# Kernel tuning notes

Measured on AMD Instinct MI355X. Metric: run time of the kernel, lower is better.

The kernel has to match this reference:

```python
import jax, jax.numpy as jnp
import numpy as np

B, T, N, D = 4, 12, 10000, 2
E = 320000
H = 64          # encoder_embed_dim
K = 2           # Chebyshev diffusion steps
P = 1           # pred_node_dim
NPRED = 12      # n_pred


def _xavier(key, shape):
    fan_in, fan_out = shape[-2], shape[-1]
    limit = np.sqrt(6.0 / (fan_in + fan_out)).astype(np.float32)
    return jax.random.uniform(key, shape, jnp.float32, -limit, limit)


def setup_inputs() -> dict:
    key = jax.random.key(0)
    ks = jax.random.split(key, 8)
    x = jax.random.normal(ks[0], (B, T, N, D), jnp.float32)
    edge_index = jax.random.randint(ks[1], (2, E), 0, N, dtype=jnp.int64)
    # positive diffusion weights, scaled ~1/avg_degree for numerical sanity
    edge_attr = jax.random.uniform(ks[2], (E,), jnp.float32) * 0.03
    W0 = _xavier(ks[3], (K, D + H, H))   # layer 0: in = node_feat + H
    b0 = jnp.zeros((H,), jnp.float32)
    W1 = _xavier(ks[4], (K, 2 * H, H))   # layer 1: in = H + H
    b1 = jnp.zeros((H,), jnp.float32)
    Wp = _xavier(ks[5], (H, P))
    bp = jnp.zeros((P,), jnp.float32)
    return {"x": x, "edge_index": edge_index, "edge_attr": edge_attr,
            "W0": W0, "b0": b0, "W1": W1, "b1": b1, "Wp": Wp, "bp": bp}


def dcrnn_layer(x, h, src, dst, ew, W, b):
    # x: [B,N,Dx], h: [B,N,H]; inp: [B,N,C] with C = Dx + H
    inp = jnp.concatenate([x, h], axis=-1)
    out = jnp.einsum('bnc,co->bno', inp, W[0])
    Hc = inp
    for k in range(1, W.shape[0]):
        # propagate: message = norm * x_j (gather at src), scatter-add at dst
        msg = ew[None, :, None] * Hc[:, src]          # [B,E,C]
        Hc = jnp.zeros_like(Hc).at[:, dst].add(msg)   # [B,N,C]
        out = out + jnp.einsum('bnc,co->bno', Hc, W[k])
    return out + b


def reference(x, edge_index, edge_attr, W0, b0, W1, b1, Wp, bp):
    src, dst = edge_index[0], edge_index[1]
    Bs, Ts, Ns, _ = x.shape
    h0 = jnp.zeros((Bs, Ns, H), x.dtype)

    def step(h, x_t):
        # layer 0: input features + recurrent state
        h1 = jax.nn.relu(dcrnn_layer(x_t, h, src, dst, edge_attr, W0, b0))
        # layer 1: x_b = h_b after layer 0, so both halves are h1
        h2 = jax.nn.relu(dcrnn_layer(h1, h1, src, dst, edge_attr, W1, b1))
        return h2, None

    xs = jnp.swapaxes(x, 0, 1)  # [T,B,N,D]
    h, _ = jax.lax.scan(step, h0, xs)
    out = h @ Wp + bp                                  # [B,N,P]
    # unsqueeze(1).repeat(1, n_pred, 1, 1)
    return jnp.broadcast_to(out[:, None], (Bs, NPRED, Ns, out.shape[-1]))
```

## Files before the change

### kernel.cpp

```cpp
#include <hip/hip_runtime.h>

#define BB 4
#define TT 12
#define NN 10000
#define DD 2
#define EE 320000
#define HH 64
#define NPREDD 12
#define TD 24
#define CAP2 1024

typedef __attribute__((ext_vector_type(8))) short bf16x8;
typedef __attribute__((ext_vector_type(4))) float f32x4;
typedef unsigned short u16;

__device__ __forceinline__ unsigned int pack2(float lo, float hi) {
    unsigned int r;
    asm("v_cvt_pk_bf16_f32 %0, %1, %2" : "=v"(r) : "v"(lo), "v"(hi));
    return r;
}
__device__ __forceinline__ float b2f(u16 u) {
    return __uint_as_float(((unsigned)u) << 16);
}

__global__ void hist_kernel(const int* __restrict__ dstv, int* __restrict__ deg) {
    int e = blockIdx.x*256 + threadIdx.x;
    if (e < EE) atomicAdd(&deg[dstv[e]], 1);
}

__global__ void scan_kernel(const int* __restrict__ deg, int* __restrict__ row_ptr,
                            int* __restrict__ cursor) {
    __shared__ int part[1024];
    int tid = threadIdx.x;
    const int CH = 10;
    int start = tid*CH;
    int s = 0;
    if (start < NN)
        for (int i=0;i<CH;i++) s += deg[start+i];
    part[tid] = s;
    __syncthreads();
    if (tid == 0) {
        int acc = 0;
        for (int i=0;i<1024;i++){ int v=part[i]; part[i]=acc; acc+=v; }
        row_ptr[NN] = acc;
    }
    __syncthreads();
    if (start < NN) {
        int acc = part[tid];
        for (int i=0;i<CH;i++){ int idx=start+i; row_ptr[idx]=acc; cursor[idx]=acc; acc+=deg[idx]; }
    }
}

__global__ void fill_kernel(const int* __restrict__ srcv, const int* __restrict__ dstv,
                            const float* __restrict__ ew, int* __restrict__ cursor,
                            int2* __restrict__ csr) {
    int e = blockIdx.x*256 + threadIdx.x;
    if (e < EE) {
        int d = dstv[e];
        int pos = atomicAdd(&cursor[d], 1);
        csr[pos] = make_int2(srcv[e], __float_as_int(ew[e]));
    }
}

__global__ void transpose_x(const float* __restrict__ x, float* __restrict__ xTb) {
    int idx = blockIdx.x*256 + threadIdx.x;
    if (idx >= BB*TT*NN*DD) return;
    int d = idx & 1;
    int n = (idx >> 1) % NN;
    int t = (idx / (NN*DD)) % TT;
    int b = idx / (TT*NN*DD);
    xTb[((size_t)n*TD + (t*DD + d))*BB + b] = x[idx];
}

__global__ __launch_bounds__(256)
void ax_gather(const float* __restrict__ xTb, const int* __restrict__ row_ptr,
               const int2* __restrict__ csr, float* __restrict__ AXb) {
    int gw = (blockIdx.x*256 + threadIdx.x) >> 6;
    if (gw >= NN) return;
    int n = gw;
    int lane = threadIdx.x & 63;
    int half = lane >> 5;
    int c = lane & 31;
    float4 acc = {0.f,0.f,0.f,0.f};
    int e0 = row_ptr[n], e1 = row_ptr[n+1];
    for (int e = e0; e < e1; e += 8) {
        int ia = e + half, ib = e + 2 + half, ic = e + 4 + half, id = e + 6 + half;
        int2 ca = csr[ia]; int2 cb = csr[ib]; int2 cc = csr[ic]; int2 cd = csr[id];
        float wa = (ia < e1) ? __int_as_float(ca.y) : 0.f;
        float wb = (ib < e1) ? __int_as_float(cb.y) : 0.f;
        float wc = (ic < e1) ? __int_as_float(cc.y) : 0.f;
        float wd = (id < e1) ? __int_as_float(cd.y) : 0.f;
        const float4 va = *(const float4*)(xTb + (size_t)ca.x*(TD*BB) + c*4);
        const float4 vb = *(const float4*)(xTb + (size_t)cb.x*(TD*BB) + c*4);
        const float4 vc = *(const float4*)(xTb + (size_t)cc.x*(TD*BB) + c*4);
        const float4 vd = *(const float4*)(xTb + (size_t)cd.x*(TD*BB) + c*4);
        acc.x = fmaf(wa, va.x, acc.x); acc.y = fmaf(wa, va.y, acc.y);
        acc.z = fmaf(wa, va.z, acc.z); acc.w = fmaf(wa, va.w, acc.w);
        acc.x = fmaf(wb, vb.x, acc.x); acc.y = fmaf(wb, vb.y, acc.y);
        acc.z = fmaf(wb, vb.z, acc.z); acc.w = fmaf(wb, vb.w, acc.w);
        acc.x = fmaf(wc, vc.x, acc.x); acc.y = fmaf(wc, vc.y, acc.y);
        acc.z = fmaf(wc, vc.z, acc.z); acc.w = fmaf(wc, vc.w, acc.w);
        acc.x = fmaf(wd, vd.x, acc.x); acc.y = fmaf(wd, vd.y, acc.y);
        acc.z = fmaf(wd, vd.z, acc.z); acc.w = fmaf(wd, vd.w, acc.w);
    }
    acc.x += __shfl_xor(acc.x, 32); acc.y += __shfl_xor(acc.y, 32);
    acc.z += __shfl_xor(acc.z, 32); acc.w += __shfl_xor(acc.w, 32);
    if (lane < TD) *(float4*)(AXb + (size_t)n*(TD*BB) + lane*4) = acc;
}

__global__ void prep_wfrag(const float* __restrict__ W0, const float* __restrict__ W1,
                           unsigned short* __restrict__ wf0, unsigned short* __restrict__ wf1) {
    int tid = blockIdx.x*256 + threadIdx.x;
    if (tid >= 2560) return;
    int layer = tid / 1280;
    int r = tid % 1280;
    int lane = r & 63;
    int ctkt = r >> 6;
    int ct = ctkt / 5, kt = ctkt % 5;
    int c = ct*16 + (lane & 15);
    int k0 = kt*32 + (lane >> 4)*8;
    unsigned short* dst = (layer ? wf1 : wf0) + r*8;
    for (int j=0;j<8;j++) {
        int k = k0 + j;
        float w = 0.f;
        if (layer == 0) {
            if (k < 64)        w = W0[(2+k)*64 + c];
            else if (k < 128)  w = W0[4224 + (2+(k-64))*64 + c];
            else if (k == 128) w = W0[c];
            else if (k == 129) w = W0[64 + c];
            else if (k == 130) w = W0[4224 + c];
            else if (k == 131) w = W0[4224 + 64 + c];
        } else {
            if (k < 64)        w = W1[k*64 + c] + W1[(k+64)*64 + c];
            else if (k < 128)  w = W1[8192 + (k-64)*64 + c] + W1[8192 + k*64 + c];
        }
        unsigned int u = __float_as_uint(w);
        unsigned int rnd = (u + 0x7fffu + ((u >> 16) & 1u)) >> 16;
        dst[j] = (unsigned short)rnd;
    }
}

template<int L0, int Z>
__global__ __launch_bounds__(512)
void layer_kernel(const u16* __restrict__ h_in,
                  const float* __restrict__ x,
                  const float* __restrict__ AXb,
                  const unsigned short* __restrict__ wf,
                  const float* __restrict__ bias,
                  const int* __restrict__ row_ptr,
                  const int2* __restrict__ csr,
                  u16* __restrict__ h_out,
                  int t)
{
    __shared__ int2 sIdx[CAP2];
    __shared__ unsigned short sA[32*168];

    int tid = threadIdx.x;
    int wave = tid >> 6, lane = tid & 63;
    int nsel = lane >> 5, laneB = (lane >> 4) & 1, cq = lane & 15;

    int pair = blockIdx.x & 1;
    int chunk = blockIdx.x >> 1;
    int n0 = chunk * 16;
    int b = pair*2 + laneB;
    int laneoff = (b*HH + cq*4)*2;

    int estart = 0, cnt = 0;
    if (!Z) {
        estart = row_ptr[n0];
        cnt = row_ptr[n0 + 16] - estart;
        int lim = cnt > CAP2 ? CAP2 : cnt;
        for (int i = tid; i < CAP2; i += 512) {
            int2 v = make_int2(0, 0);
            if (i < lim) { int2 cw = csr[estart + i]; v = make_int2(cw.x << 9, cw.y); }
            sIdx[i] = v;
        }
    }

    int ct = wave & 3, mt = wave >> 2;
    const bf16x8* wfv = (const bf16x8*)wf;
    bf16x8 bfr[5];
    #pragma unroll
    for (int kt=0; kt<5; ++kt) bfr[kt] = wfv[(ct*5+kt)*64 + lane];
    float bv = bias[ct*16 + cq];

    int n = n0 + wave*2 + nsel;
    int rowL = (wave*2 + nsel)*2 + laneB;

    ushort4 hv = make_ushort4(0,0,0,0);
    float4 acc = {0.f,0.f,0.f,0.f};
    if (!Z) {
        int eb = row_ptr[n] - estart;
        int ee = row_ptr[n+1] - estart;
        hv = *(const ushort4*)((const char*)h_in + ((size_t)n << 9) + laneoff);
        __syncthreads();
        if (cnt <= CAP2) {
            for (int e = eb; e < ee; e += 8) {
                #pragma unroll
                for (int u = 0; u < 8; ++u) {
                    int idx = e + u;
                    int2 ow = sIdx[idx & (CAP2-1)];
                    float w = (idx < ee) ? __int_as_float(ow.y) : 0.f;
                    ushort4 v = *(const ushort4*)((const char*)h_in + ow.x + laneoff);
                    acc.x = fmaf(w, b2f(v.x), acc.x);
                    acc.y = fmaf(w, b2f(v.y), acc.y);
                    acc.z = fmaf(w, b2f(v.z), acc.z);
                    acc.w = fmaf(w, b2f(v.w), acc.w);
                }
            }
        } else {
            for (int e = eb; e < ee; e += 8) {
                #pragma unroll
                for (int u = 0; u < 8; ++u) {
                    int idx = e + u;
                    int2 cw = (idx < ee) ? csr[estart + idx] : make_int2(0,0);
                    float w = (idx < ee) ? __int_as_float(cw.y) : 0.f;
                    ushort4 v = *(const ushort4*)((const char*)h_in + ((size_t)cw.x << 9) + laneoff);
                    acc.x = fmaf(w, b2f(v.x), acc.x);
                    acc.y = fmaf(w, b2f(v.y), acc.y);
                    acc.z = fmaf(w, b2f(v.z), acc.z);
                    acc.w = fmaf(w, b2f(v.w), acc.w);
                }
            }
        }
    }

    *(ushort4*)&sA[rowL*168 + cq*4] = hv;
    { uint2 pk; pk.x = pack2(acc.x, acc.y); pk.y = pack2(acc.z, acc.w);
      *(uint2*)&sA[rowL*168 + 64 + cq*4] = pk; }
    if (cq == 0) {
        uint2 pk;
        if (L0) {
            const float2 xv = *(const float2*)(x + (((size_t)b*TT + t)*NN + n)*DD);
            float ax0 = AXb[(size_t)n*(TD*BB) + (2*t)*BB + b];
            float ax1 = AXb[(size_t)n*(TD*BB) + (2*t+1)*BB + b];
            pk.x = pack2(xv.x, xv.y); pk.y = pack2(ax0, ax1);
        } else { pk.x = 0u; pk.y = 0u; }
        *(uint2*)&sA[rowL*168 + 128] = pk;
    } else if (cq < 8) {
        *(uint2*)&sA[rowL*168 + 132 + (cq-1)*4] = make_uint2(0u, 0u);
    }
    __syncthreads();

    f32x4 dacc = {0.f,0.f,0.f,0.f};
    #pragma unroll
    for (int kt=0; kt<5; ++kt) {
        bf16x8 a = *(const bf16x8*)&sA[(mt*16 + cq)*168 + kt*32 + (lane>>4)*8];
        dacc = __builtin_amdgcn_mfma_f32_16x16x32_bf16(a, bfr[kt], dacc, 0, 0, 0);
    }
    #pragma unroll
    for (int i2=0;i2<4;i2++) {
        int r = mt*16 + (lane>>4)*4 + i2;
        int nodeL = r >> 1, bo = pair*2 + (r & 1);
        float vv = fmaxf(dacc[i2] + bv, 0.f);
        unsigned pk = pack2(vv, vv);
        h_out[((size_t)(n0 + nodeL)*BB + bo)*HH + ct*16 + cq] = (u16)pk;
    }
}

__global__ void out_kernel(const u16* __restrict__ h, const float* __restrict__ Wp,
                           const float* __restrict__ bp, float* __restrict__ outp) {
    int g = blockIdx.x*256 + threadIdx.x;
    int wave = g >> 6, lane = g & 63;
    if (wave >= BB*NN) return;
    int b = wave / NN, n = wave - b*NN;
    float v = b2f(h[((size_t)n*BB + b)*HH + lane]) * Wp[lane];
    for (int off=32; off; off>>=1) v += __shfl_down(v, off);
    v = __shfl(v, 0) + bp[0];
    if (lane < NPREDD) outp[((size_t)b*NPREDD + lane)*NN + n] = v;
}

extern "C" void kernel_launch(void* const* d_in, const int* in_sizes, int n_in,
                              void* d_out, int out_size, void* d_ws, size_t ws_size,
                              hipStream_t stream) {
    const float* x   = (const float*)d_in[0];
    const int*   ei  = (const int*)d_in[1];
    const float* ew  = (const float*)d_in[2];
    const float* W0  = (const float*)d_in[3];
    const float* b0  = (const float*)d_in[4];
    const float* W1  = (const float*)d_in[5];
    const float* b1  = (const float*)d_in[6];
    const float* Wp  = (const float*)d_in[7];
    const float* bp  = (const float*)d_in[8];
    float* outp = (float*)d_out;

    char* ws = (char*)d_ws;
    size_t off = 0;
    auto alloc = [&](size_t bytes) { void* p = ws + off; off = (off + bytes + 255) & ~(size_t)255; return p; };
    u16* h      = (u16*)alloc((size_t)NN*BB*HH*2);
    u16* h1     = (u16*)alloc((size_t)NN*BB*HH*2);
    float* xTb  = (float*)alloc(((size_t)NN*TD*BB + 64)*4);
    float* AXb  = (float*)alloc((size_t)NN*TD*BB*4);
    unsigned short* wf0 = (unsigned short*)alloc(1280*8*2);
    unsigned short* wf1 = (unsigned short*)alloc(1280*8*2);
    int2*  csr  = (int2*)alloc(((size_t)EE + 16)*8);
    int* row_ptr= (int*)alloc((NN+1)*4);
    int* deg    = (int*)alloc(NN*4);
    int* cursor = (int*)alloc(NN*4);

    const int* srcv = ei;
    const int* dstv = ei + EE;

    hipMemsetAsync(deg, 0, NN*4, stream);
    hipMemsetAsync(csr + EE, 0, 16*8, stream);

    hist_kernel<<<(EE+255)/256, 256, 0, stream>>>(dstv, deg);
    scan_kernel<<<1, 1024, 0, stream>>>(deg, row_ptr, cursor);
    fill_kernel<<<(EE+255)/256, 256, 0, stream>>>(srcv, dstv, ew, cursor, csr);
    transpose_x<<<(BB*TT*NN*DD+255)/256, 256, 0, stream>>>(x, xTb);
    ax_gather<<<(NN*64+255)/256, 256, 0, stream>>>(xTb, row_ptr, csr, AXb);
    prep_wfrag<<<10, 256, 0, stream>>>(W0, W1, wf0, wf1);

    const int grid = 1250;
    layer_kernel<1,1><<<grid, 512, 0, stream>>>(h,  x, AXb, wf0, b0, row_ptr, csr, h1, 0);
    layer_kernel<0,0><<<grid, 512, 0, stream>>>(h1, nullptr, nullptr, wf1, b1, row_ptr, csr, h, 0);
    for (int t=1; t<TT; ++t) {
        layer_kernel<1,0><<<grid, 512, 0, stream>>>(h,  x, AXb, wf0, b0, row_ptr, csr, h1, t);
        layer_kernel<0,0><<<grid, 512, 0, stream>>>(h1, nullptr, nullptr, wf1, b1, row_ptr, csr, h, 0);
    }
    out_kernel<<<(BB*NN*64+255)/256, 256, 0, stream>>>(h, Wp, bp, outp);
}
```

Measured before the change: 708.1 us.

## Fuse all recurrent layer launches into one persistent cooperative kernel with grid sync

Measured after the change: 2.031 ms. +186.8%, slower.

```diff
diff --git a/kernel.cpp b/kernel.cpp
--- a/kernel.cpp
+++ b/kernel.cpp
@@ -1,4 +1,6 @@
 #include <hip/hip_runtime.h>
+#include <hip/hip_cooperative_groups.h>
+namespace cg = cooperative_groups;
 
 #define BB 4
 #define TT 12
@@ -8,7 +10,9 @@
 #define HH 64
 #define NPREDD 12
 #define TD 24
-#define CAP2 1024
+#define NCHUNK 1250
+#define NPC 8
+#define CAP 512
 
 typedef __attribute__((ext_vector_type(8))) short bf16x8;
 typedef __attribute__((ext_vector_type(4))) float f32x4;
@@ -70,42 +74,6 @@
     int t = (idx / (NN*DD)) % TT;
     int b = idx / (TT*NN*DD);
     xTb[((size_t)n*TD + (t*DD + d))*BB + b] = x[idx];
-}
-
-__global__ __launch_bounds__(256)
-void ax_gather(const float* __restrict__ xTb, const int* __restrict__ row_ptr,
-               const int2* __restrict__ csr, float* __restrict__ AXb) {
-    int gw = (blockIdx.x*256 + threadIdx.x) >> 6;
-    if (gw >= NN) return;
-    int n = gw;
-    int lane = threadIdx.x & 63;
-    int half = lane >> 5;
-    int c = lane & 31;
-    float4 acc = {0.f,0.f,0.f,0.f};
-    int e0 = row_ptr[n], e1 = row_ptr[n+1];
-    for (int e = e0; e < e1; e += 8) {
-        int ia = e + half, ib = e + 2 + half, ic = e + 4 + half, id = e + 6 + half;
-        int2 ca = csr[ia]; int2 cb = csr[ib]; int2 cc = csr[ic]; int2 cd = csr[id];
-        float wa = (ia < e1) ? __int_as_float(ca.y) : 0.f;
-        float wb = (ib < e1) ? __int_as_float(cb.y) : 0.f;
-        float wc = (ic < e1) ? __int_as_float(cc.y) : 0.f;
-        float wd = (id < e1) ? __int_as_float(cd.y) : 0.f;
-        const float4 va = *(const float4*)(xTb + (size_t)ca.x*(TD*BB) + c*4);
-        const float4 vb = *(const float4*)(xTb + (size_t)cb.x*(TD*BB) + c*4);
-        const float4 vc = *(const float4*)(xTb + (size_t)cc.x*(TD*BB) + c*4);
-        const float4 vd = *(const float4*)(xTb + (size_t)cd.x*(TD*BB) + c*4);
-        acc.x = fmaf(wa, va.x, acc.x); acc.y = fmaf(wa, va.y, acc.y);
-        acc.z = fmaf(wa, va.z, acc.z); acc.w = fmaf(wa, va.w, acc.w);
-        acc.x = fmaf(wb, vb.x, acc.x); acc.y = fmaf(wb, vb.y, acc.y);
-        acc.z = fmaf(wb, vb.z, acc.z); acc.w = fmaf(wb, vb.w, acc.w);
-        acc.x = fmaf(wc, vc.x, acc.x); acc.y = fmaf(wc, vc.y, acc.y);
-        acc.z = fmaf(wc, vc.z, acc.z); acc.w = fmaf(wc, vc.w, acc.w);
-        acc.x = fmaf(wd, vd.x, acc.x); acc.y = fmaf(wd, vd.y, acc.y);
-        acc.z = fmaf(wd, vd.z, acc.z); acc.w = fmaf(wd, vd.w, acc.w);
-    }
-    acc.x += __shfl_xor(acc.x, 32); acc.y += __shfl_xor(acc.y, 32);
-    acc.z += __shfl_xor(acc.z, 32); acc.w += __shfl_xor(acc.w, 32);
-    if (lane < TD) *(float4*)(AXb + (size_t)n*(TD*BB) + lane*4) = acc;
 }
 
 __global__ void prep_wfrag(const float* __restrict__ W0, const float* __restrict__ W1,
@@ -140,134 +108,174 @@
     }
 }
 
-template<int L0, int Z>
-__global__ __launch_bounds__(512)
-void layer_kernel(const u16* __restrict__ h_in,
-                  const float* __restrict__ x,
-                  const float* __restrict__ AXb,
-                  const unsigned short* __restrict__ wf,
-                  const float* __restrict__ bias,
-                  const int* __restrict__ row_ptr,
-                  const int2* __restrict__ csr,
-                  u16* __restrict__ h_out,
-                  int t)
+__global__ __launch_bounds__(512, 6)
+void persist2(u16* __restrict__ hA, u16* __restrict__ hB,
+              const float* __restrict__ x, const float* __restrict__ xTb,
+              float* __restrict__ AXb,
+              const unsigned short* __restrict__ wf0, const unsigned short* __restrict__ wf1,
+              const float* __restrict__ b0, const float* __restrict__ b1,
+              const int* __restrict__ row_ptr, const int2* __restrict__ csr,
+              const float* __restrict__ Wp, const float* __restrict__ bp,
+              float* __restrict__ outp)
 {
-    __shared__ int2 sIdx[CAP2];
+    __shared__ int2 sIdx[CAP];
     __shared__ unsigned short sA[32*168];
 
-    int tid = threadIdx.x;
-    int wave = tid >> 6, lane = tid & 63;
-    int nsel = lane >> 5, laneB = (lane >> 4) & 1, cq = lane & 15;
-
-    int pair = blockIdx.x & 1;
-    int chunk = blockIdx.x >> 1;
-    int n0 = chunk * 16;
-    int b = pair*2 + laneB;
-    int laneoff = (b*HH + cq*4)*2;
-
-    int estart = 0, cnt = 0;
-    if (!Z) {
-        estart = row_ptr[n0];
-        cnt = row_ptr[n0 + 16] - estart;
-        int lim = cnt > CAP2 ? CAP2 : cnt;
-        for (int i = tid; i < CAP2; i += 512) {
-            int2 v = make_int2(0, 0);
-            if (i < lim) { int2 cw = csr[estart + i]; v = make_int2(cw.x << 9, cw.y); }
-            sIdx[i] = v;
+    cg::grid_group gg = cg::this_grid();
+
+    const int tid = threadIdx.x;
+    const int wave = tid >> 6, lane = tid & 63;
+    const int bq = lane >> 4, cq = lane & 15;
+    const int G = (int)gridDim.x;
+    const int bid = (int)blockIdx.x;
+    const int laneoff = (bq*HH + cq*4)*2;
+    const int ct = wave & 3, mt = wave >> 2;
+
+    for (int ph = 0; ph < 2*TT; ++ph) {
+        const int t = ph >> 1;
+        const int L0 = !(ph & 1);
+        const u16* hin  = L0 ? hA : hB;
+        u16*       hout = L0 ? hB : hA;
+        const unsigned short* wf = L0 ? wf0 : wf1;
+        const float* bias = L0 ? b0 : b1;
+
+        for (int ck = bid; ck < NCHUNK; ck += G) {
+            const int n0 = ck * NPC;
+            const int estart = row_ptr[n0];
+            const int cnt = row_ptr[n0 + NPC] - estart;
+            const int lim = cnt > CAP ? CAP : cnt;
+            {
+                int2 v = make_int2(0, 0);
+                if (tid < lim) v = csr[estart + tid];
+                sIdx[tid] = v;
+            }
+            const int n = n0 + wave;
+            const int rowL = wave*4 + bq;
+            const int eb = row_ptr[n] - estart;
+            const int ee = row_ptr[n+1] - estart;
+
+            if (ph == 0) {
+                __syncthreads();
+                float2 axacc = {0.f, 0.f};
+                if (cnt <= CAP) {
+                    for (int e = eb; e < ee; e += 8) {
+                        #pragma unroll
+                        for (int u = 0; u < 8; ++u) {
+                            int idx = e + u;
+                            int2 cw = sIdx[idx & (CAP-1)];
+                            float w = (idx < ee) ? __int_as_float(cw.y) : 0.f;
+                            float2 v = *(const float2*)((const char*)xTb + (size_t)cw.x*(TD*BB*4) + lane*8);
+                            axacc.x = fmaf(w, v.x, axacc.x);
+                            axacc.y = fmaf(w, v.y, axacc.y);
+                        }
+                    }
+                } else {
+                    for (int e = eb; e < ee; e += 8) {
+                        #pragma unroll
+                        for (int u = 0; u < 8; ++u) {
+                            int idx = e + u;
+                            int2 cw = (idx < ee) ? csr[estart + idx] : make_int2(0,0);
+                            float w = (idx < ee) ? __int_as_float(cw.y) : 0.f;
+                            float2 v = *(const float2*)((const char*)xTb + (size_t)cw.x*(TD*BB*4) + lane*8);
+                            axacc.x = fmaf(w, v.x, axacc.x);
+                            axacc.y = fmaf(w, v.y, axacc.y);
+                        }
+                    }
+                }
+                if (lane < TD*BB/2)
+                    *(float2*)(AXb + (size_t)n*(TD*BB) + lane*2) = axacc;
+                *(ushort4*)&sA[rowL*168 + cq*4] = make_ushort4(0,0,0,0);
+                *(uint2*)&sA[rowL*168 + 64 + cq*4] = make_uint2(0u, 0u);
+                __syncthreads();
+            } else {
+                ushort4 hv = *(const ushort4*)((const char*)hin + ((size_t)n << 9) + laneoff);
+                __syncthreads();
+                float4 acc = {0.f,0.f,0.f,0.f};
+                if (cnt <= CAP) {
+                    for (int e = eb; e < ee; e += 16) {
+                        #pragma unroll
+                        for (int u = 0; u < 16; ++u) {
+                            int idx = e + u;
+                            int2 cw = sIdx[idx & (CAP-1)];
+                            float w = (idx < ee) ? __int_as_float(cw.y) : 0.f;
+                            ushort4 v = *(const ushort4*)((const char*)hin + ((size_t)cw.x << 9) + laneoff);
+                            acc.x = fmaf(w, b2f(v.x), acc.x);
+                            acc.y = fmaf(w, b2f(v.y), acc.y);
+                            acc.z = fmaf(w, b2f(v.z), acc.z);
+                            acc.w = fmaf(w, b2f(v.w), acc.w);
+                        }
+                    }
+                } else {
+                    for (int e = eb; e < ee; e += 16) {
+                        #pragma unroll
+                        for (int u = 0; u < 16; ++u) {
+                            int idx = e + u;
+                            int2 cw = (idx < ee) ? csr[estart + idx] : make_int2(0,0);
+                            float w = (idx < ee) ? __int_as_float(cw.y) : 0.f;
+                            ushort4 v = *(const ushort4*)((const char*)hin + ((size_t)cw.x << 9) + laneoff);
+                            acc.x = fmaf(w, b2f(v.x), acc.x);
+                            acc.y = fmaf(w, b2f(v.y), acc.y);
+                            acc.z = fmaf(w, b2f(v.z), acc.z);
+                            acc.w = fmaf(w, b2f(v.w), acc.w);
+                        }
+                    }
+                }
+                *(ushort4*)&sA[rowL*168 + cq*4] = hv;
+                uint2 pk; pk.x = pack2(acc.x, acc.y); pk.y = pack2(acc.z, acc.w);
+                *(uint2*)&sA[rowL*168 + 64 + cq*4] = pk;
+            }
+
+            if (cq == 0) {
+                uint2 pk;
+                if (L0) {
+                    const float2 xv = *(const float2*)(x + (((size_t)bq*TT + t)*NN + n)*DD);
+                    float ax0 = AXb[(size_t)n*(TD*BB) + (2*t)*BB + bq];
+                    float ax1 = AXb[(size_t)n*(TD*BB) + (2*t+1)*BB + bq];
+                    pk.x = pack2(xv.x, xv.y); pk.y = pack2(ax0, ax1);
+                } else { pk.x = 0u; pk.y = 0u; }
+                *(uint2*)&sA[rowL*168 + 128] = pk;
+            } else if (cq < 8) {
+                *(uint2*)&sA[rowL*168 + 132 + (cq-1)*4] = make_uint2(0u, 0u);
+            }
+
+            const bf16x8* wfv = (const bf16x8*)wf;
+            bf16x8 bfr[5];
+            #pragma unroll
+            for (int kt = 0; kt < 5; ++kt) bfr[kt] = wfv[(ct*5 + kt)*64 + lane];
+            float bv = bias[ct*16 + cq];
+
+            __syncthreads();
+
+            f32x4 dacc = {0.f,0.f,0.f,0.f};
+            #pragma unroll
+            for (int kt = 0; kt < 5; ++kt) {
+                bf16x8 a = *(const bf16x8*)&sA[(mt*16 + cq)*168 + kt*32 + bq*8];
+                dacc = __builtin_amdgcn_mfma_f32_16x16x32_bf16(a, bfr[kt], dacc, 0, 0, 0);
+            }
+            #pragma unroll
+            for (int i2 = 0; i2 < 4; ++i2) {
+                int r = mt*16 + bq*4 + i2;
+                int node = n0 + (r >> 2), b = r & 3;
+                float vv = fmaxf(dacc[i2] + bv, 0.f);
+                unsigned pk = pack2(vv, vv);
+                hout[((size_t)node*BB + b)*HH + ct*16 + cq] = (u16)pk;
+            }
+            __syncthreads();
         }
-    }
-
-    int ct = wave & 3, mt = wave >> 2;
-    const bf16x8* wfv = (const bf16x8*)wf;
-    bf16x8 bfr[5];
-    #pragma unroll
-    for (int kt=0; kt<5; ++kt) bfr[kt] = wfv[(ct*5+kt)*64 + lane];
-    float bv = bias[ct*16 + cq];
-
-    int n = n0 + wave*2 + nsel;
-    int rowL = (wave*2 + nsel)*2 + laneB;
-
-    ushort4 hv = make_ushort4(0,0,0,0);
-    float4 acc = {0.f,0.f,0.f,0.f};
-    if (!Z) {
-        int eb = row_ptr[n] - estart;
-        int ee = row_ptr[n+1] - estart;
-        hv = *(const ushort4*)((const char*)h_in + ((size_t)n << 9) + laneoff);
-        __syncthreads();
-        if (cnt <= CAP2) {
-            for (int e = eb; e < ee; e += 8) {
-                #pragma unroll
-                for (int u = 0; u < 8; ++u) {
-                    int idx = e + u;
-                    int2 ow = sIdx[idx & (CAP2-1)];
-                    float w = (idx < ee) ? __int_as_float(ow.y) : 0.f;
-                    ushort4 v = *(const ushort4*)((const char*)h_in + ow.x + laneoff);
-                    acc.x = fmaf(w, b2f(v.x), acc.x);
-                    acc.y = fmaf(w, b2f(v.y), acc.y);
-                    acc.z = fmaf(w, b2f(v.z), acc.z);
-                    acc.w = fmaf(w, b2f(v.w), acc.w);
-                }
-            }
-        } else {
-            for (int e = eb; e < ee; e += 8) {
-                #pragma unroll
-                for (int u = 0; u < 8; ++u) {
-                    int idx = e + u;
-                    int2 cw = (idx < ee) ? csr[estart + idx] : make_int2(0,0);
-                    float w = (idx < ee) ? __int_as_float(cw.y) : 0.f;
-                    ushort4 v = *(const ushort4*)((const char*)h_in + ((size_t)cw.x << 9) + laneoff);
-                    acc.x = fmaf(w, b2f(v.x), acc.x);
-                    acc.y = fmaf(w, b2f(v.y), acc.y);
-                    acc.z = fmaf(w, b2f(v.z), acc.z);
-                    acc.w = fmaf(w, b2f(v.w), acc.w);
-                }
-            }
+
+        if (ph != 2*TT - 1) gg.sync();
+    }
+
+    for (int ck = bid; ck < NCHUNK; ck += G) {
+        int n0 = ck * NPC;
+        for (int r = wave; r < NPC*BB; r += 8) {
+            int n = n0 + (r >> 2), b = r & 3;
+            float v = b2f(hA[((size_t)n*BB + b)*HH + lane]) * Wp[lane];
+            for (int off = 32; off; off >>= 1) v += __shfl_down(v, off);
+            v = __shfl(v, 0) + bp[0];
+            if (lane < NPREDD) outp[((size_t)b*NPREDD + lane)*NN + n] = v;
         }
     }
-
-    *(ushort4*)&sA[rowL*168 + cq*4] = hv;
-    { uint2 pk; pk.x = pack2(acc.x, acc.y); pk.y = pack2(acc.z, acc.w);
-      *(uint2*)&sA[rowL*168 + 64 + cq*4] = pk; }
-    if (cq == 0) {
-        uint2 pk;
-        if (L0) {
-            const float2 xv = *(const float2*)(x + (((size_t)b*TT + t)*NN + n)*DD);
-            float ax0 = AXb[(size_t)n*(TD*BB) + (2*t)*BB + b];
-            float ax1 = AXb[(size_t)n*(TD*BB) + (2*t+1)*BB + b];
-            pk.x = pack2(xv.x, xv.y); pk.y = pack2(ax0, ax1);
-        } else { pk.x = 0u; pk.y = 0u; }
-        *(uint2*)&sA[rowL*168 + 128] = pk;
-    } else if (cq < 8) {
-        *(uint2*)&sA[rowL*168 + 132 + (cq-1)*4] = make_uint2(0u, 0u);
-    }
-    __syncthreads();
-
-    f32x4 dacc = {0.f,0.f,0.f,0.f};
-    #pragma unroll
-    for (int kt=0; kt<5; ++kt) {
-        bf16x8 a = *(const bf16x8*)&sA[(mt*16 + cq)*168 + kt*32 + (lane>>4)*8];
-        dacc = __builtin_amdgcn_mfma_f32_16x16x32_bf16(a, bfr[kt], dacc, 0, 0, 0);
-    }
-    #pragma unroll
-    for (int i2=0;i2<4;i2++) {
-        int r = mt*16 + (lane>>4)*4 + i2;
-        int nodeL = r >> 1, bo = pair*2 + (r & 1);
-        float vv = fmaxf(dacc[i2] + bv, 0.f);
-        unsigned pk = pack2(vv, vv);
-        h_out[((size_t)(n0 + nodeL)*BB + bo)*HH + ct*16 + cq] = (u16)pk;
-    }
-}
-
-__global__ void out_kernel(const u16* __restrict__ h, const float* __restrict__ Wp,
-                           const float* __restrict__ bp, float* __restrict__ outp) {
-    int g = blockIdx.x*256 + threadIdx.x;
-    int wave = g >> 6, lane = g & 63;
-    if (wave >= BB*NN) return;
-    int b = wave / NN, n = wave - b*NN;
-    float v = b2f(h[((size_t)n*BB + b)*HH + lane]) * Wp[lane];
-    for (int off=32; off; off>>=1) v += __shfl_down(v, off);
-    v = __shfl(v, 0) + bp[0];
-    if (lane < NPREDD) outp[((size_t)b*NPREDD + lane)*NN + n] = v;
 }
 
 extern "C" void kernel_launch(void* const* d_in, const int* in_sizes, int n_in,
@@ -289,7 +297,7 @@
     auto alloc = [&](size_t bytes) { void* p = ws + off; off = (off + bytes + 255) & ~(size_t)255; return p; };
     u16* h      = (u16*)alloc((size_t)NN*BB*HH*2);
     u16* h1     = (u16*)alloc((size_t)NN*BB*HH*2);
-    float* xTb  = (float*)alloc(((size_t)NN*TD*BB + 64)*4);
+    float* xTb  = (float*)alloc(((size_t)NN*TD*BB + 128)*4);
     float* AXb  = (float*)alloc((size_t)NN*TD*BB*4);
     unsigned short* wf0 = (unsigned short*)alloc(1280*8*2);
     unsigned short* wf1 = (unsigned short*)alloc(1280*8*2);
@@ -302,21 +310,20 @@
     const int* dstv = ei + EE;
 
     hipMemsetAsync(deg, 0, NN*4, stream);
-    hipMemsetAsync(csr + EE, 0, 16*8, stream);
 
     hist_kernel<<<(EE+255)/256, 256, 0, stream>>>(dstv, deg);
     scan_kernel<<<1, 1024, 0, stream>>>(deg, row_ptr, cursor);
     fill_kernel<<<(EE+255)/256, 256, 0, stream>>>(srcv, dstv, ew, cursor, csr);
     transpose_x<<<(BB*TT*NN*DD+255)/256, 256, 0, stream>>>(x, xTb);
-    ax_gather<<<(NN*64+255)/256, 256, 0, stream>>>(xTb, row_ptr, csr, AXb);
     prep_wfrag<<<10, 256, 0, stream>>>(W0, W1, wf0, wf1);
 
-    const int grid = 1250;
-    layer_kernel<1,1><<<grid, 512, 0, stream>>>(h,  x, AXb, wf0, b0, row_ptr, csr, h1, 0);
-    layer_kernel<0,0><<<grid, 512, 0, stream>>>(h1, nullptr, nullptr, wf1, b1, row_ptr, csr, h, 0);
-    for (int t=1; t<TT; ++t) {
-        layer_kernel<1,0><<<grid, 512, 0, stream>>>(h,  x, AXb, wf0, b0, row_ptr, csr, h1, t);
-        layer_kernel<0,0><<<grid, 512, 0, stream>>>(h1, nullptr, nullptr, wf1, b1, row_ptr, csr, h, 0);
-    }
-    out_kernel<<<(BB*NN*64+255)/256, 256, 0, stream>>>(h, Wp, bp, outp);
-}
+    int occ = 0;
+    hipOccupancyMaxActiveBlocksPerMultiprocessor(&occ, persist2, 512, 0);
+    int cap = occ * 256;
+    int Gr = (cap >= 625) ? 625 : (cap >= 313) ? 313 : (cap >= 157) ? 157 : 79;
+
+    void* kargs[] = { (void*)&h, (void*)&h1, (void*)&x, (void*)&xTb, (void*)&AXb,
+                      (void*)&wf0, (void*)&wf1, (void*)&b0, (void*)&b1,
+                      (void*)&row_ptr, (void*)&csr, (void*)&Wp, (void*)&bp, (void*)&outp };
+    hipLaunchCooperativeKernel((void*)persist2, dim3(Gr), dim3(512), kargs, 0, stream);
+}
```
